# Performance work log

Measured on AMD Instinct MI355X. Metric: run time of the kernel, lower is better.

Reference implementation:

```python
import jax, jax.numpy as jnp
import numpy as np

B, Q, K = 4, 128, 1024
DQ, DK, DV, H = 512, 512, 512, 256
NEG_INF = -1e6


def setup_inputs() -> dict:
    key = jax.random.key(0)
    ks = jax.random.split(key, 6)
    queries = jax.random.normal(ks[0], (B, Q, DQ), dtype=jnp.float32)
    keys = jax.random.normal(ks[1], (B, K, DK), dtype=jnp.float32)
    values = jax.random.normal(ks[2], (B, K, DV), dtype=jnp.float32)
    valid_lens = jax.random.randint(ks[3], (B,), 1, K + 1, dtype=jnp.int32)
    # Learned params (Dense use_bias=False): W_q [DQ,H], W_k [DK,H], w_v [H] (Dense(1) squeezed)
    Wq = jax.random.normal(ks[4], (DQ, H), dtype=jnp.float32) / np.sqrt(DQ)
    Wk = jax.random.normal(ks[5], (DK, H), dtype=jnp.float32) / np.sqrt(DK)
    wv = jax.random.normal(jax.random.fold_in(key, 7), (H,), dtype=jnp.float32) / np.sqrt(H)
    return {"queries": queries, "keys": keys, "values": values,
            "valid_lens": valid_lens, "Wq": Wq, "Wk": Wk, "wv": wv}


def reference(queries, keys, values, valid_lens, Wq, Wk, wv):
    q = queries @ Wq                       # [B,Q,H]
    k = keys @ Wk                          # [B,K,H]
    feats = jnp.tanh(q[:, :, None, :] + k[:, None, :, :])   # [B,Q,K,H]
    scores = jnp.einsum('bqkh,h->bqk', feats, wv)            # [B,Q,K]
    mask = jnp.arange(scores.shape[-1]) < valid_lens[:, None, None]  # [B,1,K]
    scores = jnp.where(mask, scores, NEG_INF)
    attn = jax.nn.softmax(scores, axis=-1)                   # [B,Q,K]
    # dropout is identity at inference
    return attn @ values                                     # [B,Q,DV]
```

## Files before the change

### kernel.cpp

```cpp
#include <hip/hip_runtime.h>

#define Bn 4
#define Qn 128
#define Kn 1024
#define Dn 512
#define Hn 256

__device__ __forceinline__ float fast_tanh(float x) {
    float e = __expf(2.0f * x);
    return 1.0f - 2.0f * __builtin_amdgcn_rcpf(1.0f + e);
}

#define PK 32
#define PApad 68

__global__ __launch_bounds__(256) void proj_kernel(
    const float* __restrict__ queries, const float* __restrict__ keys,
    const float* __restrict__ Wq, const float* __restrict__ Wk,
    const int* __restrict__ valid_lens,
    float* __restrict__ qproj, float* __restrict__ kproj)
{
    const int blk = blockIdx.x;
    const int nt = blk & 3;
    const int mt = blk >> 2;
    const int t = threadIdx.x;
    const float* Asrc; const float* W; float* Dst;
    int m0;
    if (mt < 8) {
        m0 = mt * 64;
        Asrc = queries; W = Wq; Dst = qproj;
    } else {
        int r0 = (mt - 8) * 64;
        int b = r0 >> 10;
        if ((r0 & 1023) >= valid_lens[b]) return;
        m0 = r0;
        Asrc = keys; W = Wk; Dst = kproj;
    }
    const int n0 = nt * 64;

    __shared__ float s_a[PK][PApad];
    __shared__ float s_b[PK][64];

    const int tcol = t & 15;
    const int trow = t >> 4;

    float acc[4][4] = {{0.f}};

    for (int kt = 0; kt < 16; ++kt) {
        const int d0 = kt * PK;
        #pragma unroll
        for (int i = 0; i < 2; ++i) {
            int idx = t + i * 256;
            int row = idx >> 3;
            int c4  = idx & 7;
            float4 v = *(const float4*)(Asrc + (size_t)(m0 + row) * Dn + d0 + c4 * 4);
            s_a[c4 * 4 + 0][row] = v.x;
            s_a[c4 * 4 + 1][row] = v.y;
            s_a[c4 * 4 + 2][row] = v.z;
            s_a[c4 * 4 + 3][row] = v.w;
        }
        #pragma unroll
        for (int i = 0; i < 2; ++i) {
            int idx = t + i * 256;
            int row = idx >> 4;
            int c4  = idx & 15;
            *(float4*)&s_b[row][c4 * 4] =
                *(const float4*)(W + (size_t)(d0 + row) * Hn + n0 + c4 * 4);
        }
        __syncthreads();
        #pragma unroll 8
        for (int kk = 0; kk < PK; ++kk) {
            float4 a4 = *(const float4*)&s_a[kk][trow * 4];
            float4 b4 = *(const float4*)&s_b[kk][tcol * 4];
            float a[4] = {a4.x, a4.y, a4.z, a4.w};
            float b[4] = {b4.x, b4.y, b4.z, b4.w};
            #pragma unroll
            for (int i = 0; i < 4; ++i) {
                #pragma unroll
                for (int j = 0; j < 4; ++j)
                    acc[i][j] += a[i] * b[j];
            }
        }
        __syncthreads();
    }
    #pragma unroll
    for (int i = 0; i < 4; ++i) {
        float4 o; o.x = acc[i][0]; o.y = acc[i][1]; o.z = acc[i][2]; o.w = acc[i][3];
        *(float4*)(Dst + (size_t)(m0 + trow * 4 + i) * Hn + n0 + tcol * 4) = o;
    }
}

#define SK_KT 32
#define SK_QT 4
#define SK_PAD 260

__global__ __launch_bounds__(256) void score_kernel(
    const float* __restrict__ qproj, const float* __restrict__ kproj,
    const float* __restrict__ wv, const int* __restrict__ valid_lens,
    float* __restrict__ escores, float* __restrict__ rowsum)
{
    const int blk = blockIdx.x;
    const int kt = blk & 31;
    const int qt = (blk >> 5) & 31;
    const int b  = blk >> 10;
    const int vlen = valid_lens[b];
    const int k0 = kt * SK_KT;
    if (k0 >= vlen) return;
    const int q0 = qt * SK_QT;
    const int t = threadIdx.x;

    __shared__ float s_k[SK_KT * SK_PAD];
    __shared__ float s_q[SK_QT * Hn];
    __shared__ float s_wv[Hn];

    {
        const float4* src = reinterpret_cast<const float4*>(
            kproj + ((size_t)b * Kn + k0) * Hn);
        #pragma unroll
        for (int i = 0; i < 8; ++i) {
            int idx = t + i * 256;
            int row = idx >> 6;
            int c4  = idx & 63;
            *reinterpret_cast<float4*>(&s_k[row * SK_PAD + c4 * 4]) = src[idx];
        }
        reinterpret_cast<float4*>(s_q)[t] = reinterpret_cast<const float4*>(
            qproj + ((size_t)b * Qn + q0) * Hn)[t];
        if (t < 64)
            reinterpret_cast<float4*>(s_wv)[t] =
                reinterpret_cast<const float4*>(wv)[t];
    }
    __syncthreads();

    const int wave = t >> 6;
    const int lane = t & 63;
    const int kloc = lane & 31;
    const int hh   = (lane >> 5) * 128;

    const float4* kr = reinterpret_cast<const float4*>(&s_k[kloc * SK_PAD + hh]);
    const float4* qr = reinterpret_cast<const float4*>(&s_q[wave * Hn + hh]);
    const float4* wr = reinterpret_cast<const float4*>(&s_wv[hh]);

    float s = 0.0f;
    #pragma unroll 8
    for (int i = 0; i < 32; ++i) {
        float4 kv = kr[i];
        float4 qv = qr[i];
        float4 wq = wr[i];
        s += wq.x * fast_tanh(qv.x + kv.x);
        s += wq.y * fast_tanh(qv.y + kv.y);
        s += wq.z * fast_tanh(qv.z + kv.z);
        s += wq.w * fast_tanh(qv.w + kv.w);
    }
    s += __shfl_xor(s, 32, 64);

    const int k = k0 + (lane & 31);
    float e = 0.0f;
    if (lane < 32 && k < vlen) {
        e = __expf(s);
        escores[((size_t)b * Qn + q0 + wave) * Kn + k] = e;
    }
    #pragma unroll
    for (int off = 32; off; off >>= 1)
        e += __shfl_xor(e, off, 64);
    if (lane == 0)
        atomicAdd(&rowsum[b * Qn + q0 + wave], e);
}

#define AQT 8
__global__ __launch_bounds__(256) void av_kernel(
    const float* __restrict__ escores, const float* __restrict__ rowsum,
    const float* __restrict__ values, const int* __restrict__ valid_lens,
    float* __restrict__ out)
{
    const int blk = blockIdx.x;
    const int dq = blk & 3;
    const int qt = (blk >> 2) & 15;
    const int b  = blk >> 6;
    const int t = threadIdx.x;
    const int vlen = valid_lens[b];
    const int q0 = qt * AQT;
    const int d0 = dq * 128;
    const int col = t & 127;
    const int slice = t >> 7;

    __shared__ float s_e[AQT][Kn];
    __shared__ float s_red[128][AQT + 1];

    {
        const float4* src = reinterpret_cast<const float4*>(
            escores + (size_t)(b * Qn + q0) * Kn);
        float4* dst = reinterpret_cast<float4*>(s_e);
        #pragma unroll
        for (int i = 0; i < 8; ++i)
            dst[t + i * 256] = src[t + i * 256];
    }
    __syncthreads();

    float inv[AQT];
    #pragma unroll
    for (int j = 0; j < AQT; ++j)
        inv[j] = __builtin_amdgcn_rcpf(rowsum[b * Qn + q0 + j]);

    int kh = (vlen >> 1) + 3;
    kh &= ~3;
    if (kh > vlen) kh = vlen;
    const int ks = slice ? kh : 0;
    const int ke = slice ? vlen : kh;

    const float* vb = values + (size_t)b * Kn * Dn + d0 + col;
    float acc[AQT] = {0.f};
    int k = ks;
    for (; k + 4 <= ke; k += 4) {
        float v0 = vb[(size_t)(k + 0) * Dn];
        float v1 = vb[(size_t)(k + 1) * Dn];
        float v2 = vb[(size_t)(k + 2) * Dn];
        float v3 = vb[(size_t)(k + 3) * Dn];
        #pragma unroll
        for (int j = 0; j < AQT; ++j) {
            float4 e4 = *(const float4*)&s_e[j][k];
            acc[j] += e4.x * v0 + e4.y * v1 + e4.z * v2 + e4.w * v3;
        }
    }
    for (; k < ke; ++k) {
        float v0 = vb[(size_t)k * Dn];
        #pragma unroll
        for (int j = 0; j < AQT; ++j)
            acc[j] += s_e[j][k] * v0;
    }

    if (slice == 1) {
        #pragma unroll
        for (int j = 0; j < AQT; ++j) s_red[col][j] = acc[j];
    }
    __syncthreads();
    if (slice == 0) {
        #pragma unroll
        for (int j = 0; j < AQT; ++j) {
            float r = (acc[j] + s_red[col][j]) * inv[j];
            out[(size_t)(b * Qn + q0 + j) * Dn + d0 + col] = r;
        }
    }
}

extern "C" void kernel_launch(void* const* d_in, const int* in_sizes, int n_in,
                              void* d_out, int out_size, void* d_ws, size_t ws_size,
                              hipStream_t stream) {
    const float* queries    = (const float*)d_in[0];
    const float* keys       = (const float*)d_in[1];
    const float* values     = (const float*)d_in[2];
    const int*   valid_lens = (const int*)  d_in[3];
    const float* Wq         = (const float*)d_in[4];
    const float* Wk         = (const float*)d_in[5];
    const float* wv         = (const float*)d_in[6];
    float* out = (float*)d_out;

    float* qproj   = (float*)d_ws;
    float* kproj   = qproj + Bn * Qn * Hn;
    float* escores = kproj + Bn * Kn * Hn;
    float* rowsum  = escores + Bn * Qn * Kn;

    hipMemsetAsync(rowsum, 0, Bn * Qn * sizeof(float), stream);
    proj_kernel<<<288, 256, 0, stream>>>(queries, keys, Wq, Wk, valid_lens,
                                         qproj, kproj);
    score_kernel<<<Bn * 32 * 32, 256, 0, stream>>>(qproj, kproj, wv,
                                                   valid_lens, escores, rowsum);
    av_kernel<<<256, 256, 0, stream>>>(escores, rowsum, values, valid_lens, out);
}
```

Baseline: 181.8 us.

## Register-prefetch projection tiles, halve score tiles, split AV over K with reduction

The projection GEMM now uses 64-deep K tiles and prefetches the next tile into registers while computing the current one. The score kernel uses 16-key tiles with four lanes per key, which doubles the grid. The AV stage is split over four K chunks into partial buffers (reusing the kproj region), followed by a separate reduce-and-normalize kernel, and escores is zeroed so masked keys contribute nothing. This trades more grid parallelism and less per-block serial work for an extra launch, a 4 MB memset, a larger partial-sum round trip, and always reading all 1024 value rows even past valid_len.

```diff
diff --git a/kernel.cpp b/kernel.cpp
--- a/kernel.cpp
+++ b/kernel.cpp
@@ -11,8 +11,7 @@
     return 1.0f - 2.0f * __builtin_amdgcn_rcpf(1.0f + e);
 }
 
-#define PK 32
-#define PApad 68
+#define PBK 64
 
 __global__ __launch_bounds__(256) void proj_kernel(
     const float* __restrict__ queries, const float* __restrict__ keys,
@@ -38,50 +37,55 @@
     }
     const int n0 = nt * 64;
 
-    __shared__ float s_a[PK][PApad];
-    __shared__ float s_b[PK][64];
-
+    __shared__ float s_a[PBK][68];
+    __shared__ float s_b[PBK][64];
+
+    const int trow = t >> 4;
     const int tcol = t & 15;
-    const int trow = t >> 4;
 
     float acc[4][4] = {{0.f}};
-
-    for (int kt = 0; kt < 16; ++kt) {
-        const int d0 = kt * PK;
+    float4 ra[4], rb[4];
+
+    #pragma unroll
+    for (int i = 0; i < 4; ++i) {
+        int row = (t >> 4) + i * 16, c4 = t & 15;
+        ra[i] = *(const float4*)(Asrc + (size_t)(m0 + row) * Dn + c4 * 4);
+        rb[i] = *(const float4*)(W + (size_t)row * Hn + n0 + c4 * 4);
+    }
+
+    for (int kt = 0; kt < 8; ++kt) {
+        __syncthreads();
         #pragma unroll
-        for (int i = 0; i < 2; ++i) {
-            int idx = t + i * 256;
-            int row = idx >> 3;
-            int c4  = idx & 7;
-            float4 v = *(const float4*)(Asrc + (size_t)(m0 + row) * Dn + d0 + c4 * 4);
-            s_a[c4 * 4 + 0][row] = v.x;
-            s_a[c4 * 4 + 1][row] = v.y;
-            s_a[c4 * 4 + 2][row] = v.z;
-            s_a[c4 * 4 + 3][row] = v.w;
-        }
-        #pragma unroll
-        for (int i = 0; i < 2; ++i) {
-            int idx = t + i * 256;
-            int row = idx >> 4;
-            int c4  = idx & 15;
-            *(float4*)&s_b[row][c4 * 4] =
-                *(const float4*)(W + (size_t)(d0 + row) * Hn + n0 + c4 * 4);
+        for (int i = 0; i < 4; ++i) {
+            int row = (t >> 4) + i * 16, c4 = t & 15;
+            s_a[c4 * 4 + 0][row] = ra[i].x;
+            s_a[c4 * 4 + 1][row] = ra[i].y;
+            s_a[c4 * 4 + 2][row] = ra[i].z;
+            s_a[c4 * 4 + 3][row] = ra[i].w;
+            *(float4*)&s_b[row][c4 * 4] = rb[i];
         }
         __syncthreads();
-        #pragma unroll 8
-        for (int kk = 0; kk < PK; ++kk) {
+        if (kt < 7) {
+            const int d0n = (kt + 1) * PBK;
+            #pragma unroll
+            for (int i = 0; i < 4; ++i) {
+                int row = (t >> 4) + i * 16, c4 = t & 15;
+                ra[i] = *(const float4*)(Asrc + (size_t)(m0 + row) * Dn + d0n + c4 * 4);
+                rb[i] = *(const float4*)(W + (size_t)(d0n + row) * Hn + n0 + c4 * 4);
+            }
+        }
+        #pragma unroll 16
+        for (int kk = 0; kk < PBK; ++kk) {
             float4 a4 = *(const float4*)&s_a[kk][trow * 4];
             float4 b4 = *(const float4*)&s_b[kk][tcol * 4];
             float a[4] = {a4.x, a4.y, a4.z, a4.w};
             float b[4] = {b4.x, b4.y, b4.z, b4.w};
             #pragma unroll
-            for (int i = 0; i < 4; ++i) {
+            for (int i = 0; i < 4; ++i)
                 #pragma unroll
                 for (int j = 0; j < 4; ++j)
                     acc[i][j] += a[i] * b[j];
-            }
-        }
-        __syncthreads();
+        }
     }
     #pragma unroll
     for (int i = 0; i < 4; ++i) {
@@ -90,8 +94,7 @@
     }
 }
 
-#define SK_KT 32
-#define SK_QT 4
+#define SK_KT 16
 #define SK_PAD 260
 
 __global__ __launch_bounds__(256) void score_kernel(
@@ -100,27 +103,26 @@
     float* __restrict__ escores, float* __restrict__ rowsum)
 {
     const int blk = blockIdx.x;
-    const int kt = blk & 31;
-    const int qt = (blk >> 5) & 31;
-    const int b  = blk >> 10;
+    const int kt = blk & 63;
+    const int qt = (blk >> 6) & 31;
+    const int b  = blk >> 11;
     const int vlen = valid_lens[b];
     const int k0 = kt * SK_KT;
     if (k0 >= vlen) return;
-    const int q0 = qt * SK_QT;
+    const int q0 = qt * 4;
     const int t = threadIdx.x;
 
     __shared__ float s_k[SK_KT * SK_PAD];
-    __shared__ float s_q[SK_QT * Hn];
+    __shared__ float s_q[4 * Hn];
     __shared__ float s_wv[Hn];
 
     {
         const float4* src = reinterpret_cast<const float4*>(
             kproj + ((size_t)b * Kn + k0) * Hn);
         #pragma unroll
-        for (int i = 0; i < 8; ++i) {
+        for (int i = 0; i < 4; ++i) {
             int idx = t + i * 256;
-            int row = idx >> 6;
-            int c4  = idx & 63;
+            int row = idx >> 6, c4 = idx & 63;
             *reinterpret_cast<float4*>(&s_k[row * SK_PAD + c4 * 4]) = src[idx];
         }
         reinterpret_cast<float4*>(s_q)[t] = reinterpret_cast<const float4*>(
@@ -133,16 +135,16 @@
 
     const int wave = t >> 6;
     const int lane = t & 63;
-    const int kloc = lane & 31;
-    const int hh   = (lane >> 5) * 128;
-
-    const float4* kr = reinterpret_cast<const float4*>(&s_k[kloc * SK_PAD + hh]);
-    const float4* qr = reinterpret_cast<const float4*>(&s_q[wave * Hn + hh]);
-    const float4* wr = reinterpret_cast<const float4*>(&s_wv[hh]);
+    const int kloc = lane & 15;
+    const int hq   = lane >> 4;
+
+    const float4* kr = reinterpret_cast<const float4*>(&s_k[kloc * SK_PAD + hq * 64]);
+    const float4* qr = reinterpret_cast<const float4*>(&s_q[wave * Hn + hq * 64]);
+    const float4* wr = reinterpret_cast<const float4*>(&s_wv[hq * 64]);
 
     float s = 0.0f;
-    #pragma unroll 8
-    for (int i = 0; i < 32; ++i) {
+    #pragma unroll
+    for (int i = 0; i < 16; ++i) {
         float4 kv = kr[i];
         float4 qv = qr[i];
         float4 wq = wr[i];
@@ -151,11 +153,12 @@
         s += wq.z * fast_tanh(qv.z + kv.z);
         s += wq.w * fast_tanh(qv.w + kv.w);
     }
+    s += __shfl_xor(s, 16, 64);
     s += __shfl_xor(s, 32, 64);
 
-    const int k = k0 + (lane & 31);
+    const int k = k0 + kloc;
     float e = 0.0f;
-    if (lane < 32 && k < vlen) {
+    if (lane < 16 && k < vlen) {
         e = __expf(s);
         escores[((size_t)b * Qn + q0 + wave) * Kn + k] = e;
     }
@@ -166,80 +169,69 @@
         atomicAdd(&rowsum[b * Qn + q0 + wave], e);
 }
 
-#define AQT 8
-__global__ __launch_bounds__(256) void av_kernel(
-    const float* __restrict__ escores, const float* __restrict__ rowsum,
-    const float* __restrict__ values, const int* __restrict__ valid_lens,
-    float* __restrict__ out)
+__global__ __launch_bounds__(256) void av_part_kernel(
+    const float* __restrict__ escores, const float* __restrict__ values,
+    float* __restrict__ parts)
 {
     const int blk = blockIdx.x;
-    const int dq = blk & 3;
-    const int qt = (blk >> 2) & 15;
-    const int b  = blk >> 6;
+    const int kc = blk & 3;
+    const int dh = (blk >> 2) & 1;
+    const int qt = (blk >> 3) & 15;
+    const int b  = blk >> 7;
     const int t = threadIdx.x;
-    const int vlen = valid_lens[b];
-    const int q0 = qt * AQT;
-    const int d0 = dq * 128;
-    const int col = t & 127;
-    const int slice = t >> 7;
-
-    __shared__ float s_e[AQT][Kn];
-    __shared__ float s_red[128][AQT + 1];
-
-    {
-        const float4* src = reinterpret_cast<const float4*>(
-            escores + (size_t)(b * Qn + q0) * Kn);
-        float4* dst = reinterpret_cast<float4*>(s_e);
-        #pragma unroll
-        for (int i = 0; i < 8; ++i)
-            dst[t + i * 256] = src[t + i * 256];
+    const int q0 = qt * 8;
+    const int kb = kc * 256;
+    const int d  = dh * 256 + t;
+
+    __shared__ float s_e[8][256];
+    #pragma unroll
+    for (int i = 0; i < 2; ++i) {
+        int idx = t + i * 256;
+        int row = idx >> 6, c4 = idx & 63;
+        *(float4*)&s_e[row][c4 * 4] = *(const float4*)(
+            escores + ((size_t)(b * Qn + q0 + row)) * Kn + kb + c4 * 4);
     }
     __syncthreads();
 
-    float inv[AQT];
-    #pragma unroll
-    for (int j = 0; j < AQT; ++j)
-        inv[j] = __builtin_amdgcn_rcpf(rowsum[b * Qn + q0 + j]);
-
-    int kh = (vlen >> 1) + 3;
-    kh &= ~3;
-    if (kh > vlen) kh = vlen;
-    const int ks = slice ? kh : 0;
-    const int ke = slice ? vlen : kh;
-
-    const float* vb = values + (size_t)b * Kn * Dn + d0 + col;
-    float acc[AQT] = {0.f};
-    int k = ks;
-    for (; k + 4 <= ke; k += 4) {
+    const float* vb = values + ((size_t)b * Kn + kb) * Dn + d;
+    float acc[8] = {0.f};
+    #pragma unroll 2
+    for (int k = 0; k < 256; k += 4) {
         float v0 = vb[(size_t)(k + 0) * Dn];
         float v1 = vb[(size_t)(k + 1) * Dn];
         float v2 = vb[(size_t)(k + 2) * Dn];
         float v3 = vb[(size_t)(k + 3) * Dn];
         #pragma unroll
-        for (int j = 0; j < AQT; ++j) {
+        for (int j = 0; j < 8; ++j) {
             float4 e4 = *(const float4*)&s_e[j][k];
             acc[j] += e4.x * v0 + e4.y * v1 + e4.z * v2 + e4.w * v3;
         }
     }
-    for (; k < ke; ++k) {
-        float v0 = vb[(size_t)k * Dn];
-        #pragma unroll
-        for (int j = 0; j < AQT; ++j)
-            acc[j] += s_e[j][k] * v0;
-    }
-
-    if (slice == 1) {
-        #pragma unroll
-        for (int j = 0; j < AQT; ++j) s_red[col][j] = acc[j];
-    }
-    __syncthreads();
-    if (slice == 0) {
-        #pragma unroll
-        for (int j = 0; j < AQT; ++j) {
-            float r = (acc[j] + s_red[col][j]) * inv[j];
-            out[(size_t)(b * Qn + q0 + j) * Dn + d0 + col] = r;
-        }
-    }
+    float* pp = parts + (size_t)kc * (Bn * Qn * Dn)
+                      + ((size_t)(b * Qn + q0)) * Dn + d;
+    #pragma unroll
+    for (int j = 0; j < 8; ++j)
+        pp[(size_t)j * Dn] = acc[j];
+}
+
+__global__ __launch_bounds__(256) void reduce_kernel(
+    const float* __restrict__ parts, const float* __restrict__ rowsum,
+    float* __restrict__ out)
+{
+    const int idx = blockIdx.x * 256 + threadIdx.x;
+    const int row = (idx * 4) >> 9;
+    const float inv = __builtin_amdgcn_rcpf(rowsum[row]);
+    const float4* p = (const float4*)parts;
+    float4 a = p[idx];
+    float4 b = p[idx + 65536];
+    float4 c = p[idx + 131072];
+    float4 d = p[idx + 196608];
+    float4 o;
+    o.x = (a.x + b.x + c.x + d.x) * inv;
+    o.y = (a.y + b.y + c.y + d.y) * inv;
+    o.z = (a.z + b.z + c.z + d.z) * inv;
+    o.w = (a.w + b.w + c.w + d.w) * inv;
+    ((float4*)out)[idx] = o;
 }
 
 extern "C" void kernel_launch(void* const* d_in, const int* in_sizes, int n_in,
@@ -258,11 +250,14 @@
     float* kproj   = qproj + Bn * Qn * Hn;
     float* escores = kproj + Bn * Kn * Hn;
     float* rowsum  = escores + Bn * Qn * Kn;
-
-    hipMemsetAsync(rowsum, 0, Bn * Qn * sizeof(float), stream);
+    float* parts   = kproj;
+
+    hipMemsetAsync(escores, 0, (size_t)(Bn * Qn * Kn + Bn * Qn) * sizeof(float),
+                   stream);
     proj_kernel<<<288, 256, 0, stream>>>(queries, keys, Wq, Wk, valid_lens,
                                          qproj, kproj);
-    score_kernel<<<Bn * 32 * 32, 256, 0, stream>>>(qproj, kproj, wv,
+    score_kernel<<<Bn * 32 * 64, 256, 0, stream>>>(qproj, kproj, wv,
                                                    valid_lens, escores, rowsum);
-    av_kernel<<<256, 256, 0, stream>>>(escores, rowsum, values, valid_lens, out);
-}
+    av_part_kernel<<<512, 256, 0, stream>>>(escores, values, parts);
+    reduce_kernel<<<256, 256, 0, stream>>>(parts, rowsum, out);
+}
```

Measured after the change: 171.2 us. -5.9%, faster.
